# Kernel optimization log

Measured on AMD Instinct MI355X. Metric: run time of the kernel, lower is better.

## Reference

```python
import jax, jax.numpy as jnp
import numpy as np

EPS = 1e-05


def setup_inputs() -> dict:
    key = jax.random.key(0)
    k1, k2, k3 = jax.random.split(key, 3)
    B, S, D = 8, 4096, 1024  # batch, row(seq_len), col(d_model)
    x = jax.random.normal(k1, (B, S, D), dtype=jnp.float32)
    alpha = jnp.ones((D,), dtype=jnp.float32)
    beta = jnp.zeros((D,), dtype=jnp.float32)
    return {"x": x, "alpha": alpha, "beta": beta}


def reference(x, alpha, beta):
    # Faithful translation of LayerNorm_v2.forward, including its quirks:
    #  - statistics computed ONLY from batch element 0 (loop over x_t[0])
    #  - nonstandard running-mean recurrence: mean = (mean + data) / i
    #  - var accumulates (data - mean_i)^2 against the *updated* running mean
    #  - Bessel-style divide by (col - 1)
    # x: [B, S, D]; stats are per-row (per S), computed by streaming over D.
    B, S, D = x.shape
    data = x[0].T  # [D, S] -> loop iterates over the D (col) dimension

    def step(carry, d):
        mean, var, i = carry
        mean = (mean + d) / i          # quirky running mean
        var = var + jnp.square(d - mean)
        return (mean, var, i + 1.0), None

    init = (jnp.zeros((S,), x.dtype), jnp.zeros((S,), x.dtype),
            jnp.asarray(1.0, x.dtype))
    (mean, var, _), _ = jax.lax.scan(step, init, data)
    var = var / (D - 1)
    mean = mean[:, None]  # [S, 1]
    var = var[:, None]    # [S, 1]
    # broadcast stats from batch 0 across the whole batch, per-feature affine
    return alpha * (x - mean) / jnp.sqrt(var + EPS) + beta
```

## Files before the change

### kernel.cpp

```cpp
#include <hip/hip_runtime.h>
#include <math.h>

#define BB 8
#define SS 4096
#define DD 1024
#define EPSF 1e-5f

constexpr int ROWS    = 8;
constexpr int TPB1    = 64;
constexpr int R4      = DD / 4;
constexpr int LSTRIDE = R4 + 1;

__global__ __launch_bounds__(TPB1) void stats_kernel(
    const float* __restrict__ x,
    float* __restrict__ mean_out,
    float* __restrict__ rstd_out)
{
    __shared__ float4 tile[ROWS * LSTRIDE];

    const int tid  = threadIdx.x;
    const int row0 = blockIdx.x * ROWS;
    const float4* __restrict__ x4 =
        reinterpret_cast<const float4*>(x) + (size_t)row0 * R4;

    for (int idx = tid; idx < ROWS * R4; idx += TPB1) {
        const int r  = idx >> 8;
        const int j4 = idx & (R4 - 1);
        tile[r * LSTRIDE + j4] = x4[(size_t)r * R4 + j4];
    }
    __syncthreads();

    if (tid < ROWS) {
        float mean = 0.0f, var = 0.0f;
        const float4* rowp = &tile[tid * LSTRIDE];
        for (int jf = 0; jf < R4; ++jf) {
            const float4 v = rowp[jf];
            const float base = (float)(jf * 4);
            const float r0 = __builtin_amdgcn_rcpf(base + 1.0f);
            const float r1 = __builtin_amdgcn_rcpf(base + 2.0f);
            const float r2 = __builtin_amdgcn_rcpf(base + 3.0f);
            const float r3 = __builtin_amdgcn_rcpf(base + 4.0f);
            mean = fmaf(mean, r0, v.x * r0); { const float t = v.x - mean; var = fmaf(t, t, var); }
            mean = fmaf(mean, r1, v.y * r1); { const float t = v.y - mean; var = fmaf(t, t, var); }
            mean = fmaf(mean, r2, v.z * r2); { const float t = v.z - mean; var = fmaf(t, t, var); }
            mean = fmaf(mean, r3, v.w * r3); { const float t = v.w - mean; var = fmaf(t, t, var); }
        }
        var *= (1.0f / 1023.0f);
        mean_out[row0 + tid] = mean;
        rstd_out[row0 + tid] = rsqrtf(var + EPSF);
    }
}

constexpr int TPB2 = 256;

__global__ __launch_bounds__(TPB2) void norm_kernel(
    const float* __restrict__ x,
    const float* __restrict__ alpha,
    const float* __restrict__ beta,
    const float* __restrict__ meanp,
    const float* __restrict__ rstdp,
    float* __restrict__ out)
{
    const size_t i4 = (size_t)blockIdx.x * TPB2 + threadIdx.x;
    const int d4 = (int)(i4 & (size_t)(R4 - 1));
    const int s  = (int)((i4 >> 8) & (size_t)(SS - 1));

    const float4 xv = reinterpret_cast<const float4*>(x)[i4];
    const float4 av = reinterpret_cast<const float4*>(alpha)[d4];
    const float4 bv = reinterpret_cast<const float4*>(beta)[d4];
    const float  m  = meanp[s];
    const float  r  = rstdp[s];

    float4 o;
    o.x = fmaf(av.x * (xv.x - m), r, bv.x);
    o.y = fmaf(av.y * (xv.y - m), r, bv.y);
    o.z = fmaf(av.z * (xv.z - m), r, bv.z);
    o.w = fmaf(av.w * (xv.w - m), r, bv.w);
    reinterpret_cast<float4*>(out)[i4] = o;
}

extern "C" void kernel_launch(void* const* d_in, const int* in_sizes, int n_in,
                              void* d_out, int out_size, void* d_ws, size_t ws_size,
                              hipStream_t stream) {
    (void)in_sizes; (void)n_in; (void)out_size; (void)ws_size;
    const float* x     = (const float*)d_in[0];
    const float* alpha = (const float*)d_in[1];
    const float* beta  = (const float*)d_in[2];
    float* out     = (float*)d_out;
    float* mean_ws = (float*)d_ws;
    float* rstd_ws = mean_ws + SS;

    hipLaunchKernelGGL(stats_kernel, dim3(SS / ROWS), dim3(TPB1), 0, stream,
                       x, mean_ws, rstd_ws);

    const int n4 = (BB * SS * DD) / 4;
    hipLaunchKernelGGL(norm_kernel, dim3(n4 / TPB2), dim3(TPB2), 0, stream,
                       x, alpha, beta, mean_ws, rstd_ws, out);
}
```

Baseline: 271.0 us.

## Parallelize quirky running-mean scan across wavefront lanes using decay truncation

The stats kernel now gives each row its own wavefront. Each lane handles 16 columns and rebuilds its incoming running mean from only the previous 6 elements, which works because the recurrence multiplies the old mean by 1/i and so older terms shrink to nothing. The variance is then reduced with shuffles, which removes the serial 1024-step loop run by only 8 threads per block. The norm kernel also switches to non-temporal loads and stores and per-row indexing. The truncated recurrence is an approximation whose accuracy depends on the decay being fast, but that decay is structural and does not come from the input data.

```diff
diff --git a/kernel.cpp b/kernel.cpp
--- a/kernel.cpp
+++ b/kernel.cpp
@@ -6,54 +6,60 @@
 #define DD 1024
 #define EPSF 1e-5f
 
-constexpr int ROWS    = 8;
-constexpr int TPB1    = 64;
-constexpr int R4      = DD / 4;
-constexpr int LSTRIDE = R4 + 1;
+typedef float f32x4 __attribute__((ext_vector_type(4)));
 
-__global__ __launch_bounds__(TPB1) void stats_kernel(
+__global__ __launch_bounds__(64) void stats_kernel(
     const float* __restrict__ x,
     float* __restrict__ mean_out,
     float* __restrict__ rstd_out)
 {
-    __shared__ float4 tile[ROWS * LSTRIDE];
+    const int row = blockIdx.x;
+    const int L   = threadIdx.x;
+    const float4* __restrict__ rowp =
+        reinterpret_cast<const float4*>(x) + (size_t)row * (DD / 4);
 
-    const int tid  = threadIdx.x;
-    const int row0 = blockIdx.x * ROWS;
-    const float4* __restrict__ x4 =
-        reinterpret_cast<const float4*>(x) + (size_t)row0 * R4;
+    const float4 a0 = rowp[4 * L + 0];
+    const float4 a1 = rowp[4 * L + 1];
+    const float4 a2 = rowp[4 * L + 2];
+    const float4 a3 = rowp[4 * L + 3];
+    const float d[16] = { a0.x, a0.y, a0.z, a0.w,  a1.x, a1.y, a1.z, a1.w,
+                          a2.x, a2.y, a2.z, a2.w,  a3.x, a3.y, a3.z, a3.w };
 
-    for (int idx = tid; idx < ROWS * R4; idx += TPB1) {
-        const int r  = idx >> 8;
-        const int j4 = idx & (R4 - 1);
-        tile[r * LSTRIDE + j4] = x4[(size_t)r * R4 + j4];
+    float m = 0.0f;
+    if (L > 0) {
+        const float4 p0 = rowp[4 * L - 2];
+        const float4 p1 = rowp[4 * L - 1];
+        const float jf = (float)(16 * L);
+        float acc = p0.z;
+        acc = fmaf(acc, __builtin_amdgcn_rcpf(jf - 5.0f), p0.w);
+        acc = fmaf(acc, __builtin_amdgcn_rcpf(jf - 4.0f), p1.x);
+        acc = fmaf(acc, __builtin_amdgcn_rcpf(jf - 3.0f), p1.y);
+        acc = fmaf(acc, __builtin_amdgcn_rcpf(jf - 2.0f), p1.z);
+        acc = fmaf(acc, __builtin_amdgcn_rcpf(jf - 1.0f), p1.w);
+        m = acc * __builtin_amdgcn_rcpf(jf);
     }
-    __syncthreads();
 
-    if (tid < ROWS) {
-        float mean = 0.0f, var = 0.0f;
-        const float4* rowp = &tile[tid * LSTRIDE];
-        for (int jf = 0; jf < R4; ++jf) {
-            const float4 v = rowp[jf];
-            const float base = (float)(jf * 4);
-            const float r0 = __builtin_amdgcn_rcpf(base + 1.0f);
-            const float r1 = __builtin_amdgcn_rcpf(base + 2.0f);
-            const float r2 = __builtin_amdgcn_rcpf(base + 3.0f);
-            const float r3 = __builtin_amdgcn_rcpf(base + 4.0f);
-            mean = fmaf(mean, r0, v.x * r0); { const float t = v.x - mean; var = fmaf(t, t, var); }
-            mean = fmaf(mean, r1, v.y * r1); { const float t = v.y - mean; var = fmaf(t, t, var); }
-            mean = fmaf(mean, r2, v.z * r2); { const float t = v.z - mean; var = fmaf(t, t, var); }
-            mean = fmaf(mean, r3, v.w * r3); { const float t = v.w - mean; var = fmaf(t, t, var); }
-        }
-        var *= (1.0f / 1023.0f);
-        mean_out[row0 + tid] = mean;
-        rstd_out[row0 + tid] = rsqrtf(var + EPSF);
+    float var = 0.0f;
+    const float base = (float)(16 * L);
+#pragma unroll
+    for (int t = 0; t < 16; ++t) {
+        const float rk = __builtin_amdgcn_rcpf(base + (float)(t + 1));
+        m = (m + d[t]) * rk;
+        const float df = d[t] - m;
+        var = fmaf(df, df, var);
+    }
+
+#pragma unroll
+    for (int off = 32; off >= 1; off >>= 1) var += __shfl_down(var, off, 64);
+    const float mean_final = __shfl(m, 63, 64);
+
+    if (L == 0) {
+        mean_out[row] = mean_final;
+        rstd_out[row] = rsqrtf(var * (1.0f / 1023.0f) + EPSF);
     }
 }
 
-constexpr int TPB2 = 256;
-
-__global__ __launch_bounds__(TPB2) void norm_kernel(
+__global__ __launch_bounds__(256) void norm_kernel(
     const float* __restrict__ x,
     const float* __restrict__ alpha,
     const float* __restrict__ beta,
@@ -61,22 +67,25 @@
     const float* __restrict__ rstdp,
     float* __restrict__ out)
 {
-    const size_t i4 = (size_t)blockIdx.x * TPB2 + threadIdx.x;
-    const int d4 = (int)(i4 & (size_t)(R4 - 1));
-    const int s  = (int)((i4 >> 8) & (size_t)(SS - 1));
+    const int tid  = threadIdx.x;
+    const int brow = blockIdx.x;
+    const int s    = brow & (SS - 1);
 
-    const float4 xv = reinterpret_cast<const float4*>(x)[i4];
-    const float4 av = reinterpret_cast<const float4*>(alpha)[d4];
-    const float4 bv = reinterpret_cast<const float4*>(beta)[d4];
-    const float  m  = meanp[s];
-    const float  r  = rstdp[s];
+    const float m = meanp[s];
+    const float r = rstdp[s];
 
-    float4 o;
+    const size_t i4 = (size_t)brow * 256 + tid;
+    const f32x4 xv = __builtin_nontemporal_load(
+        reinterpret_cast<const f32x4*>(x) + i4);
+    const float4 av = reinterpret_cast<const float4*>(alpha)[tid];
+    const float4 bv = reinterpret_cast<const float4*>(beta)[tid];
+
+    f32x4 o;
     o.x = fmaf(av.x * (xv.x - m), r, bv.x);
     o.y = fmaf(av.y * (xv.y - m), r, bv.y);
     o.z = fmaf(av.z * (xv.z - m), r, bv.z);
     o.w = fmaf(av.w * (xv.w - m), r, bv.w);
-    reinterpret_cast<float4*>(out)[i4] = o;
+    __builtin_nontemporal_store(o, reinterpret_cast<f32x4*>(out) + i4);
 }
 
 extern "C" void kernel_launch(void* const* d_in, const int* in_sizes, int n_in,
@@ -90,10 +99,8 @@
     float* mean_ws = (float*)d_ws;
     float* rstd_ws = mean_ws + SS;
 
-    hipLaunchKernelGGL(stats_kernel, dim3(SS / ROWS), dim3(TPB1), 0, stream,
+    hipLaunchKernelGGL(stats_kernel, dim3(SS), dim3(64), 0, stream,
                        x, mean_ws, rstd_ws);
-
-    const int n4 = (BB * SS * DD) / 4;
-    hipLaunchKernelGGL(norm_kernel, dim3(n4 / TPB2), dim3(TPB2), 0, stream,
+    hipLaunchKernelGGL(norm_kernel, dim3(BB * SS), dim3(256), 0, stream,
                        x, alpha, beta, mean_ws, rstd_ws, out);
 }
```

After: 229.5 us. 1.18x faster.
